# Kernel tuning notes

Measured on AMD Instinct MI355X. Metric: run time of the kernel, lower is better.

Reference implementation:

```python
import jax, jax.numpy as jnp
import numpy as np

B, T, DIM, NH = 4, 2048, 1024, 16
HD = DIM // NH


def setup_inputs() -> dict:
    key = jax.random.key(0)
    ks = jax.random.split(key, 9)
    s = 0.02
    return {
        "x": jax.random.normal(ks[0], (B, T, DIM), dtype=jnp.float32),
        "Wq": jax.random.normal(ks[1], (DIM, DIM), dtype=jnp.float32) * s,
        "bq": jnp.zeros((DIM,), dtype=jnp.float32),
        "Wk": jax.random.normal(ks[2], (DIM, DIM), dtype=jnp.float32) * s,
        "bk": jnp.zeros((DIM,), dtype=jnp.float32),
        "Wv": jax.random.normal(ks[3], (DIM, DIM), dtype=jnp.float32) * s,
        "bv": jnp.zeros((DIM,), dtype=jnp.float32),
        "Wo": jax.random.normal(ks[4], (DIM, DIM), dtype=jnp.float32) * s,
        "bo": jnp.zeros((DIM,), dtype=jnp.float32),
    }


def reference(x, Wq, bq, Wk, bk, Wv, bv, Wo, bo):
    scale = HD ** -0.5
    # QKV projections (torch Linear: x @ W.T + b; here W stored as [in, out])
    q = (x @ Wq + bq).reshape(B, T, NH, HD).transpose(0, 2, 1, 3)  # [B,H,T,D]
    k = (x @ Wk + bk).reshape(B, T, NH, HD).transpose(0, 2, 1, 3)
    v = (x @ Wv + bv).reshape(B, T, NH, HD).transpose(0, 2, 1, 3)
    scores = jnp.einsum("bhqd,bhkd->bhqk", q, k) * scale  # [B,H,T,T]
    attn = jax.nn.softmax(scores, axis=-1)
    out = jnp.einsum("bhqk,bhkd->bhqd", attn, v)  # [B,H,T,D]
    out = out.transpose(0, 2, 1, 3).reshape(B, T, DIM)
    return out @ Wo + bo
```

## Files before the change

### kernel.cpp

```cpp
#include <hip/hip_runtime.h>
#include <math.h>

#define BB   4
#define TT   2048
#define DIMM 1024
#define NHH  16
#define HDD  64
#define MM   (BB * TT)

typedef unsigned short u16;
typedef unsigned int   u32;
typedef short bf16x8 __attribute__((ext_vector_type(8)));
typedef float f32x4  __attribute__((ext_vector_type(4)));

__device__ __forceinline__ u16 f2bf(float f) {
    u32 u = __float_as_uint(f);
    return (u16)((u + 0x7fffu + ((u >> 16) & 1u)) >> 16);
}

__device__ __forceinline__ f32x4 mfma16(bf16x8 a, bf16x8 b, f32x4 c) {
    return __builtin_amdgcn_mfma_f32_16x16x32_bf16(a, b, c, 0, 0, 0);
}

__device__ __forceinline__ int swz8(int row, int slot) {
    return ((slot ^ (row & 7) ^ ((row >> 3) & 7)) & 7) * 8;
}
__device__ __forceinline__ int swz4(int row, int slot) {
    return ((slot ^ (row & 3)) & 3) * 8;
}

__global__ void convert_x_bf16(const float* __restrict__ in, u16* __restrict__ out) {
    int i = (blockIdx.x * 256 + threadIdx.x) * 8;
    float4 a = *(const float4*)(in + i);
    float4 b = *(const float4*)(in + i + 4);
    u32 w0 = f2bf(a.x) | ((u32)f2bf(a.y) << 16);
    u32 w1 = f2bf(a.z) | ((u32)f2bf(a.w) << 16);
    u32 w2 = f2bf(b.x) | ((u32)f2bf(b.y) << 16);
    u32 w3 = f2bf(b.z) | ((u32)f2bf(b.w) << 16);
    uint4 o = make_uint4(w0, w1, w2, w3);
    *(uint4*)(out + i) = o;
}

__global__ void transpose_w_bf16(const float* __restrict__ W, u16* __restrict__ Wt) {
    __shared__ float tile[32][33];
    const int c  = threadIdx.x & 31;
    const int r8 = threadIdx.x >> 5;
    const int kb = blockIdx.y * 32, nb = blockIdx.x * 32;
#pragma unroll
    for (int rr = 0; rr < 4; ++rr) {
        int r = r8 + rr * 8;
        tile[r][c] = W[(kb + r) * 1024 + nb + c];
    }
    __syncthreads();
#pragma unroll
    for (int rr = 0; rr < 4; ++rr) {
        int r = r8 + rr * 8;
        Wt[(nb + r) * 1024 + kb + c] = f2bf(tile[c][r]);
    }
}

template <int OLAYOUT>
__global__ __launch_bounds__(256, 2) void gemm_bf16(
    const u16* __restrict__ A, const u16* __restrict__ Bt,
    const float* __restrict__ bias, void* __restrict__ Cout, float oscale)
{
    __shared__ u16 As[128 * 32];
    __shared__ u16 Bs[128 * 32];

    const int tid  = threadIdx.x;
    const int m0   = blockIdx.x * 128;
    const int n0   = blockIdx.y * 128;
    const int wave = tid >> 6, lane = tid & 63;
    const int wr = wave >> 1, wc = wave & 1;
    const int l15 = lane & 15, l4 = lane >> 4;

    const int r0 = tid >> 2, ks = tid & 3;
    const int r1 = r0 + 64;
    const int w0 = r0 * 32 + swz4(r0, ks);
    const int w1 = r1 * 32 + swz4(r1, ks);

    f32x4 acc[4][4];
#pragma unroll
    for (int i = 0; i < 4; ++i)
#pragma unroll
        for (int j = 0; j < 4; ++j) acc[i][j] = (f32x4){0.f, 0.f, 0.f, 0.f};

    const u16* Ar0 = A  + (m0 + r0) * 1024 + ks * 8;
    const u16* Ar1 = A  + (m0 + r1) * 1024 + ks * 8;
    const u16* Br0 = Bt + (n0 + r0) * 1024 + ks * 8;
    const u16* Br1 = Bt + (n0 + r1) * 1024 + ks * 8;

    uint4 a0 = *(const uint4*)Ar0;
    uint4 a1 = *(const uint4*)Ar1;
    uint4 b0 = *(const uint4*)Br0;
    uint4 b1 = *(const uint4*)Br1;
    *(uint4*)&As[w0] = a0; *(uint4*)&As[w1] = a1;
    *(uint4*)&Bs[w0] = b0; *(uint4*)&Bs[w1] = b1;
    __syncthreads();

    for (int kt = 0; kt < 32; ++kt) {
        if (kt < 31) {
            const int ko = (kt + 1) * 32;
            a0 = *(const uint4*)(Ar0 + ko);
            a1 = *(const uint4*)(Ar1 + ko);
            b0 = *(const uint4*)(Br0 + ko);
            b1 = *(const uint4*)(Br1 + ko);
        }
        bf16x8 af[4], bf[4];
#pragma unroll
        for (int rt = 0; rt < 4; ++rt) {
            int row = wr * 64 + rt * 16 + l15;
            af[rt] = *(const bf16x8*)&As[row * 32 + swz4(row, l4)];
            int col = wc * 64 + rt * 16 + l15;
            bf[rt] = *(const bf16x8*)&Bs[col * 32 + swz4(col, l4)];
        }
#pragma unroll
        for (int rt = 0; rt < 4; ++rt)
#pragma unroll
            for (int ct = 0; ct < 4; ++ct)
                acc[rt][ct] = mfma16(af[rt], bf[ct], acc[rt][ct]);
        __syncthreads();
        if (kt < 31) {
            *(uint4*)&As[w0] = a0; *(uint4*)&As[w1] = a1;
            *(uint4*)&Bs[w0] = b0; *(uint4*)&Bs[w1] = b1;
            __syncthreads();
        }
    }

#pragma unroll
    for (int rt = 0; rt < 4; ++rt)
#pragma unroll
        for (int ct = 0; ct < 4; ++ct) {
            int n = n0 + wc * 64 + ct * 16 + l15;
            float bn = bias[n];
            if (OLAYOUT == 2) {
                int m00 = m0 + wr * 64 + rt * 16 + l4 * 4;
                int b = m00 >> 11, t0 = m00 & 2047;
                int h = n >> 6, d = n & 63;
                ushort4 pk;
                pk.x = f2bf((acc[rt][ct][0] + bn) * oscale);
                pk.y = f2bf((acc[rt][ct][1] + bn) * oscale);
                pk.z = f2bf((acc[rt][ct][2] + bn) * oscale);
                pk.w = f2bf((acc[rt][ct][3] + bn) * oscale);
                *(ushort4*)(&((u16*)Cout)[((((b << 4) + h) * 64 + d) << 11) + t0]) = pk;
            } else {
#pragma unroll
                for (int i = 0; i < 4; ++i) {
                    int m = m0 + wr * 64 + rt * 16 + l4 * 4 + i;
                    float v = (acc[rt][ct][i] + bn) * oscale;
                    if (OLAYOUT == 0) {
                        ((float*)Cout)[m * 1024 + n] = v;
                    } else {
                        int b = m >> 11, t = m & 2047;
                        int h = n >> 6,  d = n & 63;
                        ((u16*)Cout)[(((b << 4) + h) * 2048 + t) * 64 + d] = f2bf(v);
                    }
                }
            }
        }
}

__global__ __launch_bounds__(256, 4) void attn_mfma(
    const u16* __restrict__ Qb, const u16* __restrict__ Kb,
    const u16* __restrict__ Vtg, u16* __restrict__ Ob)
{
    __shared__ u16 Ks[2][64 * 64];
    __shared__ u16 Vts[2][64 * 64];
    __shared__ u16 Ps[4][16 * 64];

    const int tid   = threadIdx.x;
    const int g     = blockIdx.x;
    const int chunk = (g & 7) * 256 + (g >> 3);
    const int bh    = chunk >> 5;
    const int q0    = (chunk & 31) * 64;
    const int b     = bh >> 4, h = bh & 15;
    const u16* Qp   = Qb + (bh * TT + q0) * HDD;
    const u16* Kp   = Kb + bh * TT * HDD;
    const u16* Vp   = Vtg + bh * TT * HDD;

    const int wave = tid >> 6, lane = tid & 63;
    const int l15 = lane & 15, l4 = lane >> 4;

    bf16x8 qf[2];
#pragma unroll
    for (int hf = 0; hf < 2; ++hf)
        qf[hf] = *(const bf16x8*)(Qp + (wave * 16 + l15) * HDD + hf * 32 + l4 * 8);

    f32x4 oacc[4];
    float mr = -INFINITY, lr = 0.f;
#pragma unroll
    for (int db = 0; db < 4; ++db) oacc[db] = (f32x4){0.f, 0.f, 0.f, 0.f};

    const int pxor = (l15 & 7) ^ ((l15 >> 3) << 2);
    u32* const Pw = (u32*)&Ps[wave][0];
    int pidx[8];
#pragma unroll
    for (int nt = 0; nt < 4; ++nt)
#pragma unroll
        for (int pp = 0; pp < 2; ++pp) {
            int k2 = nt * 16 + l4 * 4 + 2 * pp;
            int slotW = ((k2 >> 3) ^ pxor) & 7;
            pidx[nt * 2 + pp] = (l15 * 64 + slotW * 8 + (k2 & 7)) >> 1;
        }
    int pread[2];
#pragma unroll
    for (int hf = 0; hf < 2; ++hf)
        pread[hf] = l15 * 64 + ((((hf << 2) + l4) ^ pxor) & 7) * 8;

    const int r0 = tid >> 3, ds = tid & 7;
    const int r1 = r0 + 32;
    const int wo0 = r0 * 64 + swz8(r0, ds);
    const int wo1 = r1 * 64 + swz8(r1, ds);

    uint4 kr0, kr1, vr0, vr1;
    kr0 = *(const uint4*)(Kp + r0 * 64 + ds * 8);
    kr1 = *(const uint4*)(Kp + r1 * 64 + ds * 8);
    vr0 = *(const uint4*)(Vp + r0 * 2048 + ds * 8);
    vr1 = *(const uint4*)(Vp + r1 * 2048 + ds * 8);
    *(uint4*)&Ks[0][wo0]  = kr0;
    *(uint4*)&Ks[0][wo1]  = kr1;
    *(uint4*)&Vts[0][wo0] = vr0;
    *(uint4*)&Vts[0][wo1] = vr1;
    __syncthreads();

    for (int kv = 0; kv < TT / 64; ++kv) {
        const int cur = kv & 1;

        if (kv < TT / 64 - 1) {
            const u16* Kt = Kp + (kv + 1) * 64 * HDD;
            const u16* Vt = Vp + (kv + 1) * 64;
            kr0 = *(const uint4*)(Kt + r0 * 64 + ds * 8);
            kr1 = *(const uint4*)(Kt + r1 * 64 + ds * 8);
            vr0 = *(const uint4*)(Vt + r0 * 2048 + ds * 8);
            vr1 = *(const uint4*)(Vt + r1 * 2048 + ds * 8);
        }

        f32x4 sacc[4];
#pragma unroll
        for (int nt = 0; nt < 4; ++nt) sacc[nt] = (f32x4){0.f, 0.f, 0.f, 0.f};
        __builtin_amdgcn_s_setprio(1);
#pragma unroll
        for (int nt = 0; nt < 4; ++nt) {
            int krow = nt * 16 + l15;
#pragma unroll
            for (int hf = 0; hf < 2; ++hf) {
                bf16x8 kf = *(const bf16x8*)&Ks[cur][krow * 64 + swz8(krow, hf * 4 + l4)];
                sacc[nt] = mfma16(kf, qf[hf], sacc[nt]);
            }
        }
        __builtin_amdgcn_s_setprio(0);

        auto pack_pass = [&]() -> float {
            float ls = 0.f;
#pragma unroll
            for (int nt = 0; nt < 4; ++nt)
#pragma unroll
                for (int pp = 0; pp < 2; ++pp) {
                    float pa = exp2f(sacc[nt][2 * pp]     - mr);
                    float pb = exp2f(sacc[nt][2 * pp + 1] - mr);
                    ls += pa + pb;
                    u32 pk;
                    asm("v_cvt_pk_bf16_f32 %0, %1, %2" : "=v"(pk) : "v"(pa), "v"(pb));
                    Pw[pidx[nt * 2 + pp]] = pk;
                }
            return ls;
        };
        float lsum = pack_pass();
        float ls2 = lsum + __shfl_xor(lsum, 16, 64);
        ls2 += __shfl_xor(ls2, 32, 64);
        if (__builtin_expect(__any(!(ls2 < 1e30f)), 0)) {
            float mx = sacc[0][0];
#pragma unroll
            for (int nt = 0; nt < 4; ++nt)
#pragma unroll
                for (int i = 0; i < 4; ++i) mx = fmaxf(mx, sacc[nt][i]);
            mx = fmaxf(mx, __shfl_xor(mx, 16, 64));
            mx = fmaxf(mx, __shfl_xor(mx, 32, 64));
            float mnew = fmaxf(mr, mx);
            float rsc  = exp2f(mr - mnew);
            mr = mnew;
            lr *= rsc;
            float rr[4];
#pragma unroll
            for (int i = 0; i < 4; ++i) rr[i] = __shfl(rsc, l4 * 4 + i, 16);
#pragma unroll
            for (int db = 0; db < 4; ++db)
#pragma unroll
                for (int i = 0; i < 4; ++i) oacc[db][i] *= rr[i];
            lsum = pack_pass();
            ls2 = lsum + __shfl_xor(lsum, 16, 64);
            ls2 += __shfl_xor(ls2, 32, 64);
        }
        lr += ls2;

        bf16x8 pf[2];
#pragma unroll
        for (int hf = 0; hf < 2; ++hf)
            pf[hf] = *(const bf16x8*)&Ps[wave][pread[hf]];
        __builtin_amdgcn_s_setprio(1);
#pragma unroll
        for (int db = 0; db < 4; ++db) {
            int d = db * 16 + l15;
#pragma unroll
            for (int hf = 0; hf < 2; ++hf) {
                bf16x8 vf = *(const bf16x8*)&Vts[cur][d * 64 + swz8(d, hf * 4 + l4)];
                oacc[db] = mfma16(pf[hf], vf, oacc[db]);
            }
        }
        __builtin_amdgcn_s_setprio(0);

        if (kv < TT / 64 - 1) {
            const int nxt = cur ^ 1;
            *(uint4*)&Ks[nxt][wo0]  = kr0;
            *(uint4*)&Ks[nxt][wo1]  = kr1;
            *(uint4*)&Vts[nxt][wo0] = vr0;
            *(uint4*)&Vts[nxt][wo1] = vr1;
        }
        __syncthreads();
    }

    float inv[4];
#pragma unroll
    for (int i = 0; i < 4; ++i) inv[i] = 1.f / __shfl(lr, l4 * 4 + i, 16);
#pragma unroll
    for (int db = 0; db < 4; ++db)
#pragma unroll
        for (int i = 0; i < 4; ++i) {
            int t   = q0 + wave * 16 + l4 * 4 + i;
            int col = h * 64 + db * 16 + l15;
            Ob[(b * TT + t) * DIMM + col] = f2bf(oacc[db][i] * inv[i]);
        }
}

extern "C" void kernel_launch(void* const* d_in, const int* in_sizes, int n_in,
                              void* d_out, int out_size, void* d_ws, size_t ws_size,
                              hipStream_t stream)
{
    const float* x  = (const float*)d_in[0];
    const float* Wq = (const float*)d_in[1];
    const float* bq = (const float*)d_in[2];
    const float* Wk = (const float*)d_in[3];
    const float* bk = (const float*)d_in[4];
    const float* Wv = (const float*)d_in[5];
    const float* bv = (const float*)d_in[6];
    const float* Wo = (const float*)d_in[7];
    const float* bo = (const float*)d_in[8];

    u16* xb   = (u16*)d_ws;
    u16* wqt  = xb   + 8388608;
    u16* wkt  = wqt  + 1048576;
    u16* wvt  = wkt  + 1048576;
    u16* wot  = wvt  + 1048576;
    u16* qbuf = wot  + 1048576;
    u16* obuf = qbuf + 8388608;
    u16* kbuf = (u16*)d_out;
    u16* vbuf = kbuf + 8388608;

    convert_x_bf16<<<4096, 256, 0, stream>>>(x, xb);
    transpose_w_bf16<<<dim3(32, 32), 256, 0, stream>>>(Wq, wqt);
    transpose_w_bf16<<<dim3(32, 32), 256, 0, stream>>>(Wk, wkt);
    transpose_w_bf16<<<dim3(32, 32), 256, 0, stream>>>(Wv, wvt);
    transpose_w_bf16<<<dim3(32, 32), 256, 0, stream>>>(Wo, wot);

    dim3 gg(MM / 128, DIMM / 128);
    const float qscale = 0.125f * 1.44269504f;
    gemm_bf16<1><<<gg, 256, 0, stream>>>(xb, wqt, bq, qbuf, qscale);
    gemm_bf16<1><<<gg, 256, 0, stream>>>(xb, wkt, bk, kbuf, 1.0f);
    gemm_bf16<2><<<gg, 256, 0, stream>>>(xb, wvt, bv, vbuf, 1.0f);

    attn_mfma<<<BB * NHH * (TT / 64), 256, 0, stream>>>(qbuf, kbuf, vbuf, obuf);

    gemm_bf16<0><<<gg, 256, 0, stream>>>(obuf, wot, bo, d_out, 1.0f);
}
```

Before: 257.7 us.

## Keep softmax probabilities in registers, using transposed PV MFMA instead of LDS staging

The probability tile no longer goes through shared memory. Because the S accumulator layout is already transposed (K as A operand), the packed bf16 P values feed 16x16x16 MFMAs directly as the B operand, and V^T fragments are read as 4-element pieces. This removes the per-iteration LDS write/read of P and the shuffles for rescaling and normalization, and the output is written as packed 4-element stores. Launch bounds rise to 5 blocks per CU, which tightens the register budget, and the PV step now issues twice as many smaller MFMAs.

```diff
diff --git a/kernel.cpp b/kernel.cpp
--- a/kernel.cpp
+++ b/kernel.cpp
@@ -11,6 +11,7 @@
 typedef unsigned short u16;
 typedef unsigned int   u32;
 typedef short bf16x8 __attribute__((ext_vector_type(8)));
+typedef short bf16x4 __attribute__((ext_vector_type(4)));
 typedef float f32x4  __attribute__((ext_vector_type(4)));
 
 __device__ __forceinline__ u16 f2bf(float f) {
@@ -160,13 +161,12 @@
         }
 }
 
-__global__ __launch_bounds__(256, 4) void attn_mfma(
+__global__ __launch_bounds__(256, 5) void attn_mfma(
     const u16* __restrict__ Qb, const u16* __restrict__ Kb,
     const u16* __restrict__ Vtg, u16* __restrict__ Ob)
 {
     __shared__ u16 Ks[2][64 * 64];
     __shared__ u16 Vts[2][64 * 64];
-    __shared__ u16 Ps[4][16 * 64];
 
     const int tid   = threadIdx.x;
     const int g     = blockIdx.x;
@@ -189,23 +189,7 @@
     f32x4 oacc[4];
     float mr = -INFINITY, lr = 0.f;
 #pragma unroll
-    for (int db = 0; db < 4; ++db) oacc[db] = (f32x4){0.f, 0.f, 0.f, 0.f};
-
-    const int pxor = (l15 & 7) ^ ((l15 >> 3) << 2);
-    u32* const Pw = (u32*)&Ps[wave][0];
-    int pidx[8];
-#pragma unroll
-    for (int nt = 0; nt < 4; ++nt)
-#pragma unroll
-        for (int pp = 0; pp < 2; ++pp) {
-            int k2 = nt * 16 + l4 * 4 + 2 * pp;
-            int slotW = ((k2 >> 3) ^ pxor) & 7;
-            pidx[nt * 2 + pp] = (l15 * 64 + slotW * 8 + (k2 & 7)) >> 1;
-        }
-    int pread[2];
-#pragma unroll
-    for (int hf = 0; hf < 2; ++hf)
-        pread[hf] = l15 * 64 + ((((hf << 2) + l4) ^ pxor) & 7) * 8;
+    for (int dt = 0; dt < 4; ++dt) oacc[dt] = (f32x4){0.f, 0.f, 0.f, 0.f};
 
     const int r0 = tid >> 3, ds = tid & 7;
     const int r1 = r0 + 32;
@@ -250,19 +234,23 @@
         }
         __builtin_amdgcn_s_setprio(0);
 
+        bf16x4 pfr[4];
         auto pack_pass = [&]() -> float {
             float ls = 0.f;
 #pragma unroll
-            for (int nt = 0; nt < 4; ++nt)
-#pragma unroll
-                for (int pp = 0; pp < 2; ++pp) {
-                    float pa = exp2f(sacc[nt][2 * pp]     - mr);
-                    float pb = exp2f(sacc[nt][2 * pp + 1] - mr);
-                    ls += pa + pb;
-                    u32 pk;
-                    asm("v_cvt_pk_bf16_f32 %0, %1, %2" : "=v"(pk) : "v"(pa), "v"(pb));
-                    Pw[pidx[nt * 2 + pp]] = pk;
-                }
+            for (int nt = 0; nt < 4; ++nt) {
+                float p0 = exp2f(sacc[nt][0] - mr);
+                float p1 = exp2f(sacc[nt][1] - mr);
+                float p2 = exp2f(sacc[nt][2] - mr);
+                float p3 = exp2f(sacc[nt][3] - mr);
+                ls += (p0 + p1) + (p2 + p3);
+                u32 lo, hi;
+                asm("v_cvt_pk_bf16_f32 %0, %1, %2" : "=v"(lo) : "v"(p0), "v"(p1));
+                asm("v_cvt_pk_bf16_f32 %0, %1, %2" : "=v"(hi) : "v"(p2), "v"(p3));
+                union { u32 w[2]; bf16x4 v; } u;
+                u.w[0] = lo; u.w[1] = hi;
+                pfr[nt] = u.v;
+            }
             return ls;
         };
         float lsum = pack_pass();
@@ -280,31 +268,26 @@
             float rsc  = exp2f(mr - mnew);
             mr = mnew;
             lr *= rsc;
-            float rr[4];
-#pragma unroll
-            for (int i = 0; i < 4; ++i) rr[i] = __shfl(rsc, l4 * 4 + i, 16);
-#pragma unroll
-            for (int db = 0; db < 4; ++db)
-#pragma unroll
-                for (int i = 0; i < 4; ++i) oacc[db][i] *= rr[i];
+#pragma unroll
+            for (int dt = 0; dt < 4; ++dt)
+#pragma unroll
+                for (int i = 0; i < 4; ++i) oacc[dt][i] *= rsc;
             lsum = pack_pass();
             ls2 = lsum + __shfl_xor(lsum, 16, 64);
             ls2 += __shfl_xor(ls2, 32, 64);
         }
         lr += ls2;
 
-        bf16x8 pf[2];
-#pragma unroll
-        for (int hf = 0; hf < 2; ++hf)
-            pf[hf] = *(const bf16x8*)&Ps[wave][pread[hf]];
         __builtin_amdgcn_s_setprio(1);
 #pragma unroll
-        for (int db = 0; db < 4; ++db) {
-            int d = db * 16 + l15;
-#pragma unroll
-            for (int hf = 0; hf < 2; ++hf) {
-                bf16x8 vf = *(const bf16x8*)&Vts[cur][d * 64 + swz8(d, hf * 4 + l4)];
-                oacc[db] = mfma16(pf[hf], vf, oacc[db]);
+        for (int nt = 0; nt < 4; ++nt) {
+#pragma unroll
+            for (int dt = 0; dt < 4; ++dt) {
+                int row = dt * 16 + l15;
+                bf16x4 vf = *(const bf16x4*)&Vts[cur][row * 64 +
+                                swz8(row, nt * 2 + (l4 >> 1)) + (l4 & 1) * 4];
+                asm("v_mfma_f32_16x16x16_bf16 %0, %1, %2, %0"
+                    : "+v"(oacc[dt]) : "v"(vf), "v"(pfr[nt]));
             }
         }
         __builtin_amdgcn_s_setprio(0);
@@ -319,17 +302,19 @@
         __syncthreads();
     }
 
-    float inv[4];
-#pragma unroll
-    for (int i = 0; i < 4; ++i) inv[i] = 1.f / __shfl(lr, l4 * 4 + i, 16);
-#pragma unroll
-    for (int db = 0; db < 4; ++db)
-#pragma unroll
-        for (int i = 0; i < 4; ++i) {
-            int t   = q0 + wave * 16 + l4 * 4 + i;
-            int col = h * 64 + db * 16 + l15;
-            Ob[(b * TT + t) * DIMM + col] = f2bf(oacc[db][i] * inv[i]);
-        }
+    const float inv = 1.f / lr;
+    const int t = q0 + wave * 16 + l15;
+#pragma unroll
+    for (int dt = 0; dt < 4; ++dt) {
+        float o0 = oacc[dt][0] * inv, o1 = oacc[dt][1] * inv;
+        float o2 = oacc[dt][2] * inv, o3 = oacc[dt][3] * inv;
+        u32 lo, hi;
+        asm("v_cvt_pk_bf16_f32 %0, %1, %2" : "=v"(lo) : "v"(o0), "v"(o1));
+        asm("v_cvt_pk_bf16_f32 %0, %1, %2" : "=v"(hi) : "v"(o2), "v"(o3));
+        uint2 pk = make_uint2(lo, hi);
+        int col = h * 64 + dt * 16 + l4 * 4;
+        *(uint2*)&Ob[(b * TT + t) * DIMM + col] = pk;
+    }
 }
 
 extern "C" void kernel_launch(void* const* d_in, const int* in_sizes, int n_in,
```

After: 311.5 us. 1.21x slower.
